# Optimization experiments

Measured on AMD Instinct MI355X. Metric: run time of the kernel, lower is better.

## Reference

```python
import jax, jax.numpy as jnp
import numpy as np

N = 50000      # num nodes
E = 400000     # num directed edges
IN = 128       # in_channels
H = 256        # hidden_channels
OUT = 128      # out_channels
LN_EPS = 1e-5


def setup_inputs() -> dict:
    key = jax.random.key(0)
    ks = jax.random.split(key, 12)
    x = jax.random.normal(ks[0], (N, IN), jnp.float32)
    edge_index = jax.random.randint(ks[1], (2, E), 0, N, jnp.int32)

    def lin(k, fi, fo):
        return jax.random.normal(k, (fi, fo), jnp.float32) / jnp.sqrt(jnp.float32(fi))

    return {
        "x": x,
        "edge_index": edge_index,
        "W1": lin(ks[2], IN, H),  "b1": jnp.zeros((H,), jnp.float32),
        "W2": lin(ks[3], H, H),   "b2": jnp.zeros((H,), jnp.float32),
        "W3": lin(ks[4], H, H),   "b3": jnp.zeros((H,), jnp.float32),
        "W4": lin(ks[5], H, OUT), "b4": jnp.zeros((OUT,), jnp.float32),
        "g1": jnp.ones((H,), jnp.float32),   "be1": jnp.zeros((H,), jnp.float32),
        "g2": jnp.ones((H,), jnp.float32),   "be2": jnp.zeros((H,), jnp.float32),
        "g3": jnp.ones((H,), jnp.float32),   "be3": jnp.zeros((H,), jnp.float32),
        "g4": jnp.ones((OUT,), jnp.float32), "be4": jnp.zeros((OUT,), jnp.float32),
    }


def layer_norm(h, g, b):
    m = jnp.mean(h, axis=-1, keepdims=True)
    v = jnp.mean(jnp.square(h - m), axis=-1, keepdims=True)
    return (h - m) * jax.lax.rsqrt(v + LN_EPS) * g + b


def gcn_conv(h, W, b, src, dst, dinv):
    # PyG GCNConv: add self-loops, norm = deg^-1/2[src] * deg^-1/2[dst]
    h = h @ W                                             # [N, F_out]
    norm = (dinv[src] * dinv[dst])[:, None]               # [E, 1]
    msg = h[src] * norm                                   # [E, F_out] irregular gather
    agg = jax.ops.segment_sum(msg, dst, num_segments=N)   # scatter-add
    agg = agg + h * jnp.square(dinv)[:, None]             # self-loop term
    return agg + b


def reference(x, edge_index, W1, b1, W2, b2, W3, b3, W4, b4,
              g1, be1, g2, be2, g3, be3, g4, be4):
    src, dst = edge_index[0], edge_index[1]
    # degree (incl. self-loop) from destination index, as in PyG gcn_norm
    deg = jax.ops.segment_sum(jnp.ones((E,), jnp.float32), dst, num_segments=N) + 1.0
    dinv = jax.lax.rsqrt(deg)

    h = gcn_conv(x, W1, b1, src, dst, dinv)
    h = jax.nn.relu(layer_norm(h, g1, be1))   # dropout = identity (eval)
    h = gcn_conv(h, W2, b2, src, dst, dinv)
    h = jax.nn.relu(layer_norm(h, g2, be2))
    h = gcn_conv(h, W3, b3, src, dst, dinv)
    h = jax.nn.relu(layer_norm(h, g3, be3))
    h = gcn_conv(h, W4, b4, src, dst, dinv)
    h = layer_norm(h, g4, be4)
    return h
```

## Files before the change

### kernel.cpp

```cpp
#include <hip/hip_runtime.h>

#define NN 50000
#define NEDGE 400000
#define MPAD 50048
#define NB 196
constexpr float LN_EPS = 1e-5f;

typedef __attribute__((ext_vector_type(8))) short bf16x8;
typedef __attribute__((ext_vector_type(4))) float f32x4;

__device__ __forceinline__ unsigned short f2bf(float f) {
  unsigned int u = __float_as_uint(f);
  u += 0x7FFFu + ((u >> 16) & 1u);
  return (unsigned short)(u >> 16);
}
__device__ __forceinline__ float bf2f(unsigned short u) {
  return __uint_as_float(((unsigned int)u) << 16);
}

__global__ void k_count(const int* __restrict__ dst, int* __restrict__ cnt) {
  int e = blockIdx.x * blockDim.x + threadIdx.x;
  if (e < NEDGE) atomicAdd(&cnt[dst[e]], 1);
}

__global__ __launch_bounds__(256) void k_bsum(const int* __restrict__ cnt,
                                              int* __restrict__ bsum,
                                              float* __restrict__ dinv) {
  const int i = blockIdx.x * 256 + threadIdx.x;
  int v = 0;
  if (i < NN) {
    v = cnt[i];
    dinv[i] = rsqrtf((float)v + 1.0f);
  }
  int s = v;
#pragma unroll
  for (int off = 32; off > 0; off >>= 1) s += __shfl_xor(s, off);
  __shared__ int wsum[4];
  if ((threadIdx.x & 63) == 0) wsum[threadIdx.x >> 6] = s;
  __syncthreads();
  if (threadIdx.x == 0) bsum[blockIdx.x] = wsum[0] + wsum[1] + wsum[2] + wsum[3];
}

__global__ __launch_bounds__(256) void k_bscan(const int* __restrict__ bsum,
                                               int* __restrict__ boff,
                                               int* __restrict__ rowptr) {
  const int t = threadIdx.x;
  const int lane = t & 63, wid = t >> 6;
  int v = (t < NB) ? bsum[t] : 0;
  int inc = v;
  for (int off = 1; off < 64; off <<= 1) {
    int y = __shfl_up(inc, off);
    if (lane >= off) inc += y;
  }
  __shared__ int wsum[4], woff[4];
  if (lane == 63) wsum[wid] = inc;
  __syncthreads();
  if (t == 0) {
    int run = 0;
    for (int w = 0; w < 4; ++w) { woff[w] = run; run += wsum[w]; }
    rowptr[NN] = NEDGE;
  }
  __syncthreads();
  if (t < NB) boff[t] = woff[wid] + inc - v;
}

__global__ __launch_bounds__(256) void k_bapply(const int* __restrict__ cnt,
                                                const int* __restrict__ boff,
                                                int* __restrict__ rowptr) {
  const int t = threadIdx.x;
  const int i = blockIdx.x * 256 + t;
  const int lane = t & 63, wid = t >> 6;
  int v = (i < NN) ? cnt[i] : 0;
  int inc = v;
  for (int off = 1; off < 64; off <<= 1) {
    int y = __shfl_up(inc, off);
    if (lane >= off) inc += y;
  }
  __shared__ int wsum[4], woff[4];
  if (lane == 63) wsum[wid] = inc;
  __syncthreads();
  if (t == 0) {
    int run = 0;
    for (int w = 0; w < 4; ++w) { woff[w] = run; run += wsum[w]; }
  }
  __syncthreads();
  if (i < NN) rowptr[i] = boff[blockIdx.x] + woff[wid] + inc - v;
}

__global__ void k_fill(const int* __restrict__ src, const int* __restrict__ dst,
                       const int* __restrict__ rowptr, int* __restrict__ fill,
                       int* __restrict__ eidx) {
  int e = blockIdx.x * blockDim.x + threadIdx.x;
  if (e >= NEDGE) return;
  const int d = dst[e];
  const int p = rowptr[d] + atomicAdd(&fill[d], 1);
  eidx[p] = src[e];
}

__global__ __launch_bounds__(256) void k_wconv_all(
    const float* __restrict__ W1, const float* __restrict__ W2,
    const float* __restrict__ W3, const float* __restrict__ W4,
    unsigned short* __restrict__ Wt1, unsigned short* __restrict__ Wt2,
    unsigned short* __restrict__ Wt3, unsigned short* __restrict__ Wt4) {
  const int b = blockIdx.x;
  const int n = threadIdx.x;
  if (b < 128) {
    Wt1[(size_t)n * 128 + b] = f2bf(W1[(size_t)b * 256 + n]);
  } else if (b < 384) {
    const int k = b - 128;
    Wt2[(size_t)n * 256 + k] = f2bf(W2[(size_t)k * 256 + n]);
  } else if (b < 640) {
    const int k = b - 384;
    Wt3[(size_t)n * 256 + k] = f2bf(W3[(size_t)k * 256 + n]);
  } else {
    const int k = b - 640;
    if (n < 128) Wt4[(size_t)n * 256 + k] = f2bf(W4[(size_t)k * 128 + n]);
  }
}

__global__ void k_xconv(const float* __restrict__ in, unsigned short* __restrict__ out) {
  const int i = blockIdx.x * blockDim.x + threadIdx.x;
  if (i >= NN * 32) return;
  float4 v = reinterpret_cast<const float4*>(in)[i];
  ushort4 o; o.x = f2bf(v.x); o.y = f2bf(v.y); o.z = f2bf(v.z); o.w = f2bf(v.w);
  reinterpret_cast<ushort4*>(out)[i] = o;
}

template<int F, bool OUTBF>
__global__ __launch_bounds__(256) void k_gather(const int* __restrict__ rowptr,
                                                const int* __restrict__ eidx,
                                                const float* __restrict__ dinv,
                                                const unsigned short* __restrict__ h,
                                                void* __restrict__ outv) {
  constexpr int VE = F / 64;
  const int n = blockIdx.x * 4 + (threadIdx.x >> 6);
  if (n >= NN) return;
  const int lane = threadIdx.x & 63;
  const float dn = dinv[n];
  const int beg = rowptr[n], end = rowptr[n + 1];

  float acc[VE];

  auto loadrow = [&](int r, float* v) {
    if constexpr (VE == 4) {
      ushort4 t = *reinterpret_cast<const ushort4*>(h + (size_t)r * F + lane * 4);
      v[0] = bf2f(t.x); v[1] = bf2f(t.y); v[2] = bf2f(t.z); v[3] = bf2f(t.w);
    } else {
      ushort2 t = *reinterpret_cast<const ushort2*>(h + (size_t)r * F + lane * 2);
      v[0] = bf2f(t.x); v[1] = bf2f(t.y);
    }
  };

  float v0[VE], v1[VE];
  loadrow(n, v0);
  const float sw = dn * dn;
#pragma unroll
  for (int i = 0; i < VE; ++i) acc[i] = v0[i] * sw;

  int e = beg;
  for (; e + 1 < end; e += 2) {
    const int s0 = eidx[e], s1 = eidx[e + 1];
    const float w0 = dinv[s0] * dn;
    const float w1 = dinv[s1] * dn;
    loadrow(s0, v0);
    loadrow(s1, v1);
#pragma unroll
    for (int i = 0; i < VE; ++i) {
      acc[i] = fmaf(v0[i], w0, acc[i]);
      acc[i] = fmaf(v1[i], w1, acc[i]);
    }
  }
  if (e < end) {
    const int s0 = eidx[e];
    const float w0 = dinv[s0] * dn;
    loadrow(s0, v0);
#pragma unroll
    for (int i = 0; i < VE; ++i) acc[i] = fmaf(v0[i], w0, acc[i]);
  }

  if constexpr (OUTBF) {
    unsigned short* out = (unsigned short*)outv;
    if constexpr (VE == 4) {
      ushort4 o; o.x = f2bf(acc[0]); o.y = f2bf(acc[1]); o.z = f2bf(acc[2]); o.w = f2bf(acc[3]);
      *reinterpret_cast<ushort4*>(out + (size_t)n * F + lane * 4) = o;
    } else {
      ushort2 o; o.x = f2bf(acc[0]); o.y = f2bf(acc[1]);
      *reinterpret_cast<ushort2*>(out + (size_t)n * F + lane * 2) = o;
    }
  } else {
    float* out = (float*)outv;
    if constexpr (VE == 4) {
      float4 o; o.x = acc[0]; o.y = acc[1]; o.z = acc[2]; o.w = acc[3];
      *reinterpret_cast<float4*>(out + (size_t)n * F + lane * 4) = o;
    } else {
      float2 o; o.x = acc[0]; o.y = acc[1];
      *reinterpret_cast<float2*>(out + (size_t)n * F + lane * 2) = o;
    }
  }
}

template<int K, int N, bool LNFUSE>
__global__ __launch_bounds__(256) void k_mgemm(const unsigned short* __restrict__ A,
                                               const unsigned short* __restrict__ Bt,
                                               const float* __restrict__ bias,
                                               const float* __restrict__ gamma,
                                               const float* __restrict__ beta,
                                               unsigned short* __restrict__ out) {
  constexpr int NT = N / 64;
  constexpr int KS = K / 32;
  __shared__ __align__(16) unsigned short As[64 * K];

  const int tid = threadIdx.x;
  const int lane = tid & 63;
  const int w = tid >> 6;
  const int m0 = blockIdx.x * 64;

#pragma unroll
  for (int i = 0; i < KS; ++i) {
    const int o = (i * 256 + tid) * 16;
    const int row = o / (2 * K);
    const int inb = o % (2 * K);
    uint4 val = *reinterpret_cast<const uint4*>(
        (const char*)A + (size_t)(m0 + row) * (2 * K) + inb);
    const int dsto = o ^ ((row & 7) << 4);
    *reinterpret_cast<uint4*>((char*)As + dsto) = val;
  }
  __syncthreads();

  f32x4 acc[4][NT];
#pragma unroll
  for (int mt = 0; mt < 4; ++mt)
#pragma unroll
    for (int nt = 0; nt < NT; ++nt) acc[mt][nt] = (f32x4){0.f, 0.f, 0.f, 0.f};

  const int nw0 = w * (N / 4);
  const int arow = lane & 15;
  const int kgrp = (lane >> 4) * 8;

  for (int ks = 0; ks < KS; ++ks) {
    bf16x8 af[4];
#pragma unroll
    for (int mt = 0; mt < 4; ++mt) {
      const int r = mt * 16 + arow;
      int boff = (r * K + ks * 32 + kgrp) * 2;
      boff ^= (r & 7) << 4;
      af[mt] = *reinterpret_cast<const bf16x8*>((const char*)As + boff);
    }
    bf16x8 bfr[NT];
#pragma unroll
    for (int nt = 0; nt < NT; ++nt) {
      const int n = nw0 + nt * 16 + arow;
      bfr[nt] = *reinterpret_cast<const bf16x8*>(Bt + (size_t)n * K + ks * 32 + kgrp);
    }
#pragma unroll
    for (int mt = 0; mt < 4; ++mt)
#pragma unroll
      for (int nt = 0; nt < NT; ++nt)
        acc[mt][nt] = __builtin_amdgcn_mfma_f32_16x16x32_bf16(af[mt], bfr[nt], acc[mt][nt], 0, 0, 0);
  }

  const int g = lane >> 4;
  const int cl = lane & 15;

  if constexpr (LNFUSE) {
    float gv[NT], bev[NT];
#pragma unroll
    for (int nt = 0; nt < NT; ++nt) {
      const int c = nw0 + nt * 16 + cl;
      const float bv = bias[c];
      gv[nt] = gamma[c];
      bev[nt] = beta[c];
#pragma unroll
      for (int mt = 0; mt < 4; ++mt)
#pragma unroll
        for (int reg = 0; reg < 4; ++reg) acc[mt][nt][reg] += bv;
    }
    __shared__ float sS[4][64];
    __shared__ float sQ[4][64];
    float ps[4][4], pq[4][4];
#pragma unroll
    for (int mt = 0; mt < 4; ++mt) {
#pragma unroll
      for (int reg = 0; reg < 4; ++reg) {
        float s = 0.f, q = 0.f;
#pragma unroll
        for (int nt = 0; nt < NT; ++nt) {
          const float v = acc[mt][nt][reg];
          s += v; q = fmaf(v, v, q);
        }
#pragma unroll
        for (int off = 1; off < 16; off <<= 1) {
          s += __shfl_xor(s, off);
          q += __shfl_xor(q, off);
        }
        ps[mt][reg] = s; pq[mt][reg] = q;
      }
    }
    if (cl == 0) {
#pragma unroll
      for (int mt = 0; mt < 4; ++mt)
#pragma unroll
        for (int reg = 0; reg < 4; ++reg) {
          sS[w][mt * 16 + g * 4 + reg] = ps[mt][reg];
          sQ[w][mt * 16 + g * 4 + reg] = pq[mt][reg];
        }
    }
    __syncthreads();
#pragma unroll
    for (int mt = 0; mt < 4; ++mt) {
#pragma unroll
      for (int reg = 0; reg < 4; ++reg) {
        const int rr = mt * 16 + g * 4 + reg;
        const int r = m0 + rr;
        const float S = sS[0][rr] + sS[1][rr] + sS[2][rr] + sS[3][rr];
        const float Q = sQ[0][rr] + sQ[1][rr] + sQ[2][rr] + sQ[3][rr];
        const float mean = S * (1.0f / N);
        const float var = Q * (1.0f / N) - mean * mean;
        const float inv = rsqrtf(var + LN_EPS);
        if (r < NN) {
#pragma unroll
          for (int nt = 0; nt < NT; ++nt) {
            const int c = nw0 + nt * 16 + cl;
            const float o = fmaxf((acc[mt][nt][reg] - mean) * inv * gv[nt] + bev[nt], 0.f);
            out[(size_t)r * N + c] = f2bf(o);
          }
        }
      }
    }
  } else {
#pragma unroll
    for (int mt = 0; mt < 4; ++mt) {
#pragma unroll
      for (int nt = 0; nt < NT; ++nt) {
        const int c = nw0 + nt * 16 + cl;
#pragma unroll
        for (int reg = 0; reg < 4; ++reg) {
          const int r = m0 + mt * 16 + g * 4 + reg;
          if (r < NN) out[(size_t)r * N + c] = f2bf(acc[mt][nt][reg]);
        }
      }
    }
  }
}

__global__ void k_ln_final(float* __restrict__ io, const float* __restrict__ bias,
                           const float* __restrict__ g, const float* __restrict__ be) {
  const int row = blockIdx.x * 4 + (threadIdx.x >> 6);
  if (row >= NN) return;
  const int lane = threadIdx.x & 63;
  float2* rowp = reinterpret_cast<float2*>(io + (size_t)row * 128);
  float2 v = rowp[lane];
  const float2 bv = reinterpret_cast<const float2*>(bias)[lane];
  const float a0 = v.x + bv.x, a1 = v.y + bv.y;
  float s = a0 + a1, q = a0 * a0 + a1 * a1;
#pragma unroll
  for (int off = 32; off > 0; off >>= 1) {
    s += __shfl_xor(s, off);
    q += __shfl_xor(q, off);
  }
  const float mean = s * (1.0f / 128.0f);
  const float var = q * (1.0f / 128.0f) - mean * mean;
  const float inv = rsqrtf(var + LN_EPS);
  const float2 gv = reinterpret_cast<const float2*>(g)[lane];
  const float2 bev = reinterpret_cast<const float2*>(be)[lane];
  float2 o;
  o.x = (a0 - mean) * inv * gv.x + bev.x;
  o.y = (a1 - mean) * inv * gv.y + bev.y;
  rowp[lane] = o;
}

extern "C" void kernel_launch(void* const* d_in, const int* in_sizes, int n_in,
                              void* d_out, int out_size, void* d_ws, size_t ws_size,
                              hipStream_t stream) {
  const float* x   = (const float*)d_in[0];
  const int*   ei  = (const int*)d_in[1];
  const float* W1  = (const float*)d_in[2];
  const float* b1  = (const float*)d_in[3];
  const float* W2  = (const float*)d_in[4];
  const float* b2  = (const float*)d_in[5];
  const float* W3  = (const float*)d_in[6];
  const float* b3  = (const float*)d_in[7];
  const float* W4  = (const float*)d_in[8];
  const float* b4  = (const float*)d_in[9];
  const float* g1  = (const float*)d_in[10];
  const float* be1 = (const float*)d_in[11];
  const float* g2  = (const float*)d_in[12];
  const float* be2 = (const float*)d_in[13];
  const float* g3  = (const float*)d_in[14];
  const float* be3 = (const float*)d_in[15];
  const float* g4  = (const float*)d_in[16];
  const float* be4 = (const float*)d_in[17];

  const int* src = ei;
  const int* dst = ei + NEDGE;

  char* ws = (char*)d_ws;
  int*   cnt    = (int*)(ws + 0);
  int*   fill   = (int*)(ws + 204800);
  int*   rowptr = (int*)(ws + 409600);
  float* dinv   = (float*)(ws + 614400);
  int*   bsum   = (int*)(ws + 819200);
  int*   boff   = (int*)(ws + 823296);
  int*   eidx   = (int*)(ws + 827392);
  unsigned short* Wt1 = (unsigned short*)(ws + 2465792);
  unsigned short* Wt2 = (unsigned short*)(ws + 2531328);
  unsigned short* Wt3 = (unsigned short*)(ws + 2662400);
  unsigned short* Wt4 = (unsigned short*)(ws + 2793472);
  unsigned short* xB  = (unsigned short*)(ws + 2859008);
  unsigned short* aggB = (unsigned short*)(ws + 15671296);
  unsigned short* hB   = (unsigned short*)(ws + 41295872);
  unsigned short* t4B  = (unsigned short*)(ws + 66920448);
  float* out = (float*)d_out;

  const int MB = (NN + 63) / 64;

  hipMemsetAsync(cnt, 0, 409600, stream);
  k_count<<<(NEDGE + 255) / 256, 256, 0, stream>>>(dst, cnt);
  k_bsum<<<NB, 256, 0, stream>>>(cnt, bsum, dinv);
  k_bscan<<<1, 256, 0, stream>>>(bsum, boff, rowptr);
  k_bapply<<<NB, 256, 0, stream>>>(cnt, boff, rowptr);
  k_fill<<<(NEDGE + 255) / 256, 256, 0, stream>>>(src, dst, rowptr, fill, eidx);
  k_wconv_all<<<896, 256, 0, stream>>>(W1, W2, W3, W4, Wt1, Wt2, Wt3, Wt4);
  k_xconv<<<(NN * 32 + 255) / 256, 256, 0, stream>>>(x, xB);

  k_gather<128, true><<<(NN + 3) / 4, 256, 0, stream>>>(rowptr, eidx, dinv, xB, aggB);
  k_mgemm<128, 256, true><<<MB, 256, 0, stream>>>(aggB, Wt1, b1, g1, be1, hB);

  k_gather<256, true><<<(NN + 3) / 4, 256, 0, stream>>>(rowptr, eidx, dinv, hB, aggB);
  k_mgemm<256, 256, true><<<MB, 256, 0, stream>>>(aggB, Wt2, b2, g2, be2, hB);

  k_gather<256, true><<<(NN + 3) / 4, 256, 0, stream>>>(rowptr, eidx, dinv, hB, aggB);
  k_mgemm<256, 256, true><<<MB, 256, 0, stream>>>(aggB, Wt3, b3, g3, be3, hB);

  k_mgemm<256, 128, false><<<MB, 256, 0, stream>>>(hB, Wt4, nullptr, nullptr, nullptr, t4B);
  k_gather<128, false><<<(NN + 3) / 4, 256, 0, stream>>>(rowptr, eidx, dinv, t4B, out);
  k_ln_final<<<(NN + 3) / 4, 256, 0, stream>>>(out, b4, g4, be4);
}
```

Baseline: 335.6 us.

## Pack edge weights into CSR, widen gather to 16B lanes, fuse final LayerNorm

The CSR fill step now stores each edge as a (src, dinv[src]*dinv[dst]) pair, so the gather kernels no longer do a dependent dinv lookup per edge. The gather is restructured so each lane loads 16 bytes and several nodes share one wavefront (4 nodes per wave at F=128, 2 at F=256). The loop is driven by a wavefront ballot, giving fewer, wider memory transactions. The final bias plus LayerNorm is fused into the last gather, which removes a separate kernel and a full read and write of the fp32 output. The cost is larger edge metadata (8 bytes per edge) and possible divergence between nodes of different degree sharing a wave.

```diff
diff --git a/kernel.cpp b/kernel.cpp
--- a/kernel.cpp
+++ b/kernel.cpp
@@ -8,6 +8,7 @@
 
 typedef __attribute__((ext_vector_type(8))) short bf16x8;
 typedef __attribute__((ext_vector_type(4))) float f32x4;
+typedef __attribute__((ext_vector_type(8))) unsigned short ushort8v;
 
 __device__ __forceinline__ unsigned short f2bf(float f) {
   unsigned int u = __float_as_uint(f);
@@ -88,13 +89,14 @@
 }
 
 __global__ void k_fill(const int* __restrict__ src, const int* __restrict__ dst,
-                       const int* __restrict__ rowptr, int* __restrict__ fill,
-                       int* __restrict__ eidx) {
+                       const float* __restrict__ dinv, const int* __restrict__ rowptr,
+                       int* __restrict__ fill, int2* __restrict__ eidx2) {
   int e = blockIdx.x * blockDim.x + threadIdx.x;
   if (e >= NEDGE) return;
   const int d = dst[e];
+  const int s = src[e];
   const int p = rowptr[d] + atomicAdd(&fill[d], 1);
-  eidx[p] = src[e];
+  eidx2[p] = make_int2(s, __float_as_int(dinv[s] * dinv[d]));
 }
 
 __global__ __launch_bounds__(256) void k_wconv_all(
@@ -126,76 +128,94 @@
   reinterpret_cast<ushort4*>(out)[i] = o;
 }
 
-template<int F, bool OUTBF>
-__global__ __launch_bounds__(256) void k_gather(const int* __restrict__ rowptr,
-                                                const int* __restrict__ eidx,
-                                                const float* __restrict__ dinv,
-                                                const unsigned short* __restrict__ h,
-                                                void* __restrict__ outv) {
-  constexpr int VE = F / 64;
-  const int n = blockIdx.x * 4 + (threadIdx.x >> 6);
-  if (n >= NN) return;
-  const int lane = threadIdx.x & 63;
-  const float dn = dinv[n];
-  const int beg = rowptr[n], end = rowptr[n + 1];
-
-  float acc[VE];
-
-  auto loadrow = [&](int r, float* v) {
-    if constexpr (VE == 4) {
-      ushort4 t = *reinterpret_cast<const ushort4*>(h + (size_t)r * F + lane * 4);
-      v[0] = bf2f(t.x); v[1] = bf2f(t.y); v[2] = bf2f(t.z); v[3] = bf2f(t.w);
-    } else {
-      ushort2 t = *reinterpret_cast<const ushort2*>(h + (size_t)r * F + lane * 2);
-      v[0] = bf2f(t.x); v[1] = bf2f(t.y);
-    }
-  };
-
-  float v0[VE], v1[VE];
-  loadrow(n, v0);
+template<int F, int NPW, int MODE>
+__global__ __launch_bounds__(256) void k_gather(
+    const int* __restrict__ rowptr, const int2* __restrict__ eidx2,
+    const float* __restrict__ dinv, const unsigned short* __restrict__ h,
+    void* __restrict__ outv, const float* __restrict__ bias,
+    const float* __restrict__ gamma, const float* __restrict__ beta) {
+  constexpr int LPN = 64 / NPW;
+  static_assert(F / LPN == 8, "16B per lane");
+  const int tid = threadIdx.x;
+  const int lane = tid & 63;
+  const int sub = lane / LPN;
+  const int slane = lane % LPN;
+  const int n = blockIdx.x * (4 * NPW) + (tid >> 6) * NPW + sub;
+  const bool valid = n < NN;
+
+  int e = 0, end = 0;
+  float dn = 0.f;
+  if (valid) {
+    dn = dinv[n];
+    e = rowptr[n];
+    end = rowptr[n + 1];
+  }
+
+  float acc[8];
+  ushort8v r0 = (ushort8v)0, r1 = (ushort8v)0;
+  if (valid) r0 = *reinterpret_cast<const ushort8v*>(h + (size_t)n * F + slane * 8);
   const float sw = dn * dn;
 #pragma unroll
-  for (int i = 0; i < VE; ++i) acc[i] = v0[i] * sw;
-
-  int e = beg;
-  for (; e + 1 < end; e += 2) {
-    const int s0 = eidx[e], s1 = eidx[e + 1];
-    const float w0 = dinv[s0] * dn;
-    const float w1 = dinv[s1] * dn;
-    loadrow(s0, v0);
-    loadrow(s1, v1);
-#pragma unroll
-    for (int i = 0; i < VE; ++i) {
-      acc[i] = fmaf(v0[i], w0, acc[i]);
-      acc[i] = fmaf(v1[i], w1, acc[i]);
-    }
-  }
-  if (e < end) {
-    const int s0 = eidx[e];
-    const float w0 = dinv[s0] * dn;
-    loadrow(s0, v0);
-#pragma unroll
-    for (int i = 0; i < VE; ++i) acc[i] = fmaf(v0[i], w0, acc[i]);
-  }
-
-  if constexpr (OUTBF) {
-    unsigned short* out = (unsigned short*)outv;
-    if constexpr (VE == 4) {
-      ushort4 o; o.x = f2bf(acc[0]); o.y = f2bf(acc[1]); o.z = f2bf(acc[2]); o.w = f2bf(acc[3]);
-      *reinterpret_cast<ushort4*>(out + (size_t)n * F + lane * 4) = o;
-    } else {
-      ushort2 o; o.x = f2bf(acc[0]); o.y = f2bf(acc[1]);
-      *reinterpret_cast<ushort2*>(out + (size_t)n * F + lane * 2) = o;
-    }
+  for (int j = 0; j < 8; ++j) acc[j] = bf2f(r0[j]) * sw;
+  r0 = (ushort8v)0;
+
+  while (__ballot(e < end)) {
+    float w0 = 0.f, w1 = 0.f;
+    if (e < end) {
+      const int2 p = eidx2[e];
+      w0 = __int_as_float(p.y);
+      r0 = *reinterpret_cast<const ushort8v*>(h + (size_t)p.x * F + slane * 8);
+    }
+    if (e + 1 < end) {
+      const int2 p = eidx2[e + 1];
+      w1 = __int_as_float(p.y);
+      r1 = *reinterpret_cast<const ushort8v*>(h + (size_t)p.x * F + slane * 8);
+    }
+#pragma unroll
+    for (int j = 0; j < 8; ++j)
+      acc[j] += w0 * bf2f(r0[j]) + w1 * bf2f(r1[j]);
+    e += 2;
+  }
+
+  if (!valid) return;
+
+  if constexpr (MODE == 0) {
+    ushort8v o;
+#pragma unroll
+    for (int j = 0; j < 8; ++j) o[j] = f2bf(acc[j]);
+    *reinterpret_cast<ushort8v*>((unsigned short*)outv + (size_t)n * F + slane * 8) = o;
   } else {
-    float* out = (float*)outv;
-    if constexpr (VE == 4) {
-      float4 o; o.x = acc[0]; o.y = acc[1]; o.z = acc[2]; o.w = acc[3];
-      *reinterpret_cast<float4*>(out + (size_t)n * F + lane * 4) = o;
-    } else {
-      float2 o; o.x = acc[0]; o.y = acc[1];
-      *reinterpret_cast<float2*>(out + (size_t)n * F + lane * 2) = o;
-    }
+    const float4 b0 = *reinterpret_cast<const float4*>(bias + slane * 8);
+    const float4 b1 = *reinterpret_cast<const float4*>(bias + slane * 8 + 4);
+    acc[0] += b0.x; acc[1] += b0.y; acc[2] += b0.z; acc[3] += b0.w;
+    acc[4] += b1.x; acc[5] += b1.y; acc[6] += b1.z; acc[7] += b1.w;
+    float s = 0.f, q = 0.f;
+#pragma unroll
+    for (int j = 0; j < 8; ++j) { s += acc[j]; q = fmaf(acc[j], acc[j], q); }
+#pragma unroll
+    for (int off = 1; off < 16; off <<= 1) {
+      s += __shfl_xor(s, off);
+      q += __shfl_xor(q, off);
+    }
+    const float mean = s * (1.0f / 128.0f);
+    const float var = q * (1.0f / 128.0f) - mean * mean;
+    const float inv = rsqrtf(var + LN_EPS);
+    const float4 g0 = *reinterpret_cast<const float4*>(gamma + slane * 8);
+    const float4 g1 = *reinterpret_cast<const float4*>(gamma + slane * 8 + 4);
+    const float4 e0 = *reinterpret_cast<const float4*>(beta + slane * 8);
+    const float4 e1 = *reinterpret_cast<const float4*>(beta + slane * 8 + 4);
+    float4 o0, o1;
+    o0.x = (acc[0] - mean) * inv * g0.x + e0.x;
+    o0.y = (acc[1] - mean) * inv * g0.y + e0.y;
+    o0.z = (acc[2] - mean) * inv * g0.z + e0.z;
+    o0.w = (acc[3] - mean) * inv * g0.w + e0.w;
+    o1.x = (acc[4] - mean) * inv * g1.x + e1.x;
+    o1.y = (acc[5] - mean) * inv * g1.y + e1.y;
+    o1.z = (acc[6] - mean) * inv * g1.z + e1.z;
+    o1.w = (acc[7] - mean) * inv * g1.w + e1.w;
+    float* out = (float*)outv + (size_t)n * 128 + slane * 8;
+    *reinterpret_cast<float4*>(out) = o0;
+    *reinterpret_cast<float4*>(out + 4) = o1;
   }
 }
 
@@ -341,32 +361,6 @@
       }
     }
   }
-}
-
-__global__ void k_ln_final(float* __restrict__ io, const float* __restrict__ bias,
-                           const float* __restrict__ g, const float* __restrict__ be) {
-  const int row = blockIdx.x * 4 + (threadIdx.x >> 6);
-  if (row >= NN) return;
-  const int lane = threadIdx.x & 63;
-  float2* rowp = reinterpret_cast<float2*>(io + (size_t)row * 128);
-  float2 v = rowp[lane];
-  const float2 bv = reinterpret_cast<const float2*>(bias)[lane];
-  const float a0 = v.x + bv.x, a1 = v.y + bv.y;
-  float s = a0 + a1, q = a0 * a0 + a1 * a1;
-#pragma unroll
-  for (int off = 32; off > 0; off >>= 1) {
-    s += __shfl_xor(s, off);
-    q += __shfl_xor(q, off);
-  }
-  const float mean = s * (1.0f / 128.0f);
-  const float var = q * (1.0f / 128.0f) - mean * mean;
-  const float inv = rsqrtf(var + LN_EPS);
-  const float2 gv = reinterpret_cast<const float2*>(g)[lane];
-  const float2 bev = reinterpret_cast<const float2*>(be)[lane];
-  float2 o;
-  o.x = (a0 - mean) * inv * gv.x + bev.x;
-  o.y = (a1 - mean) * inv * gv.y + bev.y;
-  rowp[lane] = o;
 }
 
 extern "C" void kernel_launch(void* const* d_in, const int* in_sizes, int n_in,
@@ -401,15 +395,15 @@
   float* dinv   = (float*)(ws + 614400);
   int*   bsum   = (int*)(ws + 819200);
   int*   boff   = (int*)(ws + 823296);
-  int*   eidx   = (int*)(ws + 827392);
-  unsigned short* Wt1 = (unsigned short*)(ws + 2465792);
-  unsigned short* Wt2 = (unsigned short*)(ws + 2531328);
-  unsigned short* Wt3 = (unsigned short*)(ws + 2662400);
-  unsigned short* Wt4 = (unsigned short*)(ws + 2793472);
-  unsigned short* xB  = (unsigned short*)(ws + 2859008);
-  unsigned short* aggB = (unsigned short*)(ws + 15671296);
-  unsigned short* hB   = (unsigned short*)(ws + 41295872);
-  unsigned short* t4B  = (unsigned short*)(ws + 66920448);
+  int2*  eidx2  = (int2*)(ws + 827392);
+  unsigned short* Wt1 = (unsigned short*)(ws + 4030464);
+  unsigned short* Wt2 = (unsigned short*)(ws + 4096000);
+  unsigned short* Wt3 = (unsigned short*)(ws + 4227072);
+  unsigned short* Wt4 = (unsigned short*)(ws + 4358144);
+  unsigned short* xB  = (unsigned short*)(ws + 4423680);
+  unsigned short* aggB = (unsigned short*)(ws + 17235968);
+  unsigned short* hB   = (unsigned short*)(ws + 42860544);
+  unsigned short* t4B  = (unsigned short*)(ws + 68485120);
   float* out = (float*)d_out;
 
   const int MB = (NN + 63) / 64;
@@ -419,20 +413,19 @@
   k_bsum<<<NB, 256, 0, stream>>>(cnt, bsum, dinv);
   k_bscan<<<1, 256, 0, stream>>>(bsum, boff, rowptr);
   k_bapply<<<NB, 256, 0, stream>>>(cnt, boff, rowptr);
-  k_fill<<<(NEDGE + 255) / 256, 256, 0, stream>>>(src, dst, rowptr, fill, eidx);
+  k_fill<<<(NEDGE + 255) / 256, 256, 0, stream>>>(src, dst, dinv, rowptr, fill, eidx2);
   k_wconv_all<<<896, 256, 0, stream>>>(W1, W2, W3, W4, Wt1, Wt2, Wt3, Wt4);
   k_xconv<<<(NN * 32 + 255) / 256, 256, 0, stream>>>(x, xB);
 
-  k_gather<128, true><<<(NN + 3) / 4, 256, 0, stream>>>(rowptr, eidx, dinv, xB, aggB);
+  k_gather<128, 4, 0><<<(NN + 15) / 16, 256, 0, stream>>>(rowptr, eidx2, dinv, xB, aggB, nullptr, nullptr, nullptr);
   k_mgemm<128, 256, true><<<MB, 256, 0, stream>>>(aggB, Wt1, b1, g1, be1, hB);
 
-  k_gather<256, true><<<(NN + 3) / 4, 256, 0, stream>>>(rowptr, eidx, dinv, hB, aggB);
+  k_gather<256, 2, 0><<<(NN + 7) / 8, 256, 0, stream>>>(rowptr, eidx2, dinv, hB, aggB, nullptr, nullptr, nullptr);
   k_mgemm<256, 256, true><<<MB, 256, 0, stream>>>(aggB, Wt2, b2, g2, be2, hB);
 
-  k_gather<256, true><<<(NN + 3) / 4, 256, 0, stream>>>(rowptr, eidx, dinv, hB, aggB);
+  k_gather<256, 2, 0><<<(NN + 7) / 8, 256, 0, stream>>>(rowptr, eidx2, dinv, hB, aggB, nullptr, nullptr, nullptr);
   k_mgemm<256, 256, true><<<MB, 256, 0, stream>>>(aggB, Wt3, b3, g3, be3, hB);
 
   k_mgemm<256, 128, false><<<MB, 256, 0, stream>>>(hB, Wt4, nullptr, nullptr, nullptr, t4B);
-  k_gather<128, false><<<(NN + 3) / 4, 256, 0, stream>>>(rowptr, eidx, dinv, t4B, out);
-  k_ln_final<<<(NN + 3) / 4, 256, 0, stream>>>(out, b4, g4, be4);
-}
+  k_gather<128, 4, 1><<<(NN + 15) / 16, 256, 0, stream>>>(rowptr, eidx2, dinv, t4B, out, b4, g4, be4);
+}
```

Result: faster. 297.8 us (-11.2%).
